# Kernel tuning notes

Hardware: AMD Instinct MI355X
Metric: run time of the kernel (lower is better)

The kernel has to match this reference:

```python
import jax, jax.numpy as jnp
import numpy as np

NUM_NODES = 50000
NUM_HYPEREDGES = 20000
NNZ = 1600000
IN_DIM = 256
OUT_DIM = 128


def setup_inputs() -> dict:
    key = jax.random.key(0)
    k1, k2, k3, k4, k5 = jax.random.split(key, 5)
    x = jax.random.normal(k1, (NUM_NODES, IN_DIM), dtype=jnp.float32)
    node_idx = jax.random.randint(k2, (NNZ,), 0, NUM_NODES)
    edge_idx = jax.random.randint(k3, (NNZ,), 0, NUM_HYPEREDGES)
    hyperedge_index = jnp.stack([node_idx, edge_idx], axis=0)  # [2, nnz]
    # glorot-style init for HypergraphConv's internal Linear (bias=False)
    scale = np.sqrt(6.0 / (IN_DIM + OUT_DIM)).astype(np.float32)
    lin_weight = jax.random.uniform(k4, (IN_DIM, OUT_DIM), dtype=jnp.float32,
                                    minval=-scale, maxval=scale)
    bias = jnp.zeros((OUT_DIM,), dtype=jnp.float32)
    return {"x_node_features": x, "lin_weight": lin_weight, "bias": bias,
            "hyperedge_index": hyperedge_index}


def reference(x_node_features, lin_weight, bias, hyperedge_index):
    src = hyperedge_index[0]   # node ids   [nnz]
    edge = hyperedge_index[1]  # hyperedge ids [nnz]
    ones = jnp.ones_like(src, dtype=x_node_features.dtype)

    # X Theta
    xw = x_node_features @ lin_weight  # [N, F_out]

    # D^{-1}: node degree (hyperedge weights default to 1)
    deg_n = jax.ops.segment_sum(ones, src, num_segments=NUM_NODES)
    d_inv = jnp.where(deg_n > 0, 1.0 / deg_n, 0.0)
    # B^{-1}: hyperedge cardinality
    deg_e = jax.ops.segment_sum(ones, edge, num_segments=NUM_HYPEREDGES)
    b_inv = jnp.where(deg_e > 0, 1.0 / deg_e, 0.0)

    # node -> hyperedge: m_e = B_e^{-1} * sum_{i in e} (X Theta)_i
    m_e = jax.ops.segment_sum(xw[src], edge, num_segments=NUM_HYPEREDGES)
    m_e = m_e * b_inv[:, None]  # [E, F_out]

    # hyperedge -> node: out_i = D_i^{-1} * sum_{e ni i} m_e
    out = jax.ops.segment_sum(m_e[edge], src, num_segments=NUM_NODES)
    out = out * d_inv[:, None] + bias  # [N, F_out]

    # ReLU + mean pool over nodes
    return jnp.mean(jax.nn.relu(out), axis=0)  # [F_out]
```

## Files before the change

kernel.cpp:

```cpp
#include <hip/hip_runtime.h>

#define NUM_N 50000
#define NUM_E 20000
#define IN_DIM 256
#define OUT_DIM 128
#define NBE 1250
#define NBN 1563
#define NCLS 8
#define ECAPC 256
#define NCAPC 192
#define SCAT_CHUNK 4096
#define NGEMM 782
#define XSCALE 16.0f

typedef unsigned short ushort_t;
typedef unsigned int uint_t;
typedef __attribute__((ext_vector_type(8))) short short8_t;
typedef __attribute__((ext_vector_type(4))) float f32x4_t;

__device__ __forceinline__ int clamp8(int q) { return min(max(q, -127), 127); }
__device__ __forceinline__ int lo8(uint_t u) { return (int)(signed char)(u & 0xff); }
__device__ __forceinline__ int hi8(uint_t u) { return ((int)(short)(ushort_t)u) >> 8; }
__device__ __forceinline__ ushort_t f2bf(float f) {
    uint_t u = __float_as_uint(f);
    u += 0x7fffu + ((u >> 16) & 1u);
    return (ushort_t)(u >> 16);
}

__global__ void init_kernel(int* __restrict__ gcur_e, int* __restrict__ gcur_n,
                            float* __restrict__ macc) {
    int t = blockIdx.x * 1024 + threadIdx.x;
    if (t < NCLS * NBE) gcur_e[t] = t * ECAPC;
    if (t < NCLS * NBN) gcur_n[t] = t * NCAPC;
    if (t < 128) macc[t] = 0.f;
}

__global__ __launch_bounds__(256) void gemm_scatter_kernel(
        const float* __restrict__ x, const float* __restrict__ w,
        char* __restrict__ xw, int nrows,
        const int* __restrict__ node_idx, const int* __restrict__ edge_idx, int nnz,
        int* __restrict__ gcur_e, int* __restrict__ gcur_n,
        uint_t* __restrict__ stag_e, uint_t* __restrict__ stag_n) {
    __shared__ int smem[5632];
    int tid = threadIdx.x;

    if (blockIdx.x >= NGEMM) {
        int* lh    = smem;
        int* lbase = smem + 2813;
        int cls = blockIdx.x & (NCLS - 1);
        int bid = blockIdx.x - NGEMM;
        int nblk = gridDim.x - NGEMM;
        for (int cbase = bid * SCAT_CHUNK; cbase < nnz; cbase += nblk * SCAT_CHUNK) {
            int cend = min(cbase + SCAT_CHUNK, nnz);
            for (int i = tid; i < NBE + NBN; i += 256) lh[i] = 0;
            __syncthreads();
            for (int i = cbase + tid; i < cend; i += 256) {
                atomicAdd(&lh[edge_idx[i] >> 4], 1);
                atomicAdd(&lh[NBE + (node_idx[i] >> 5)], 1);
            }
            __syncthreads();
            for (int i = tid; i < NBE; i += 256) {
                int c = lh[i];
                lbase[i] = c ? atomicAdd(&gcur_e[cls * NBE + i], c) : 0;
            }
            for (int i = tid; i < NBN; i += 256) {
                int c = lh[NBE + i];
                lbase[NBE + i] = c ? atomicAdd(&gcur_n[cls * NBN + i], c) : 0;
            }
            __syncthreads();
            for (int i = tid; i < NBE + NBN; i += 256) lh[i] = 0;
            __syncthreads();
            for (int i = cbase + tid; i < cend; i += 256) {
                int v = node_idx[i];
                int e = edge_idx[i];
                uint_t pk = ((uint_t)v << 16) | (uint_t)e;
                int be = e >> 4;
                int bn = v >> 5;
                int pe = lbase[be] + atomicAdd(&lh[be], 1);
                if (pe < (cls * NBE + be + 1) * ECAPC) stag_e[pe] = pk;
                int pn = lbase[NBE + bn] + atomicAdd(&lh[NBE + bn], 1);
                if (pn < (cls * NBN + bn + 1) * NCAPC) stag_n[pn] = pk;
            }
            __syncthreads();
        }
        return;
    }

    ushort_t* Wt = (ushort_t*)smem;
    int lane = tid & 63;
    int wv = tid >> 6;
    int R = blockIdx.x * 64 + wv * 16;
    int fr = lane & 15;
    int kb = lane >> 4;
    f32x4_t acc[8];
#pragma unroll
    for (int c = 0; c < 8; ++c) acc[c] = (f32x4_t){0.f, 0.f, 0.f, 0.f};
    int arow = min(R + fr, nrows - 1);
    const float* ap = x + (size_t)arow * IN_DIM + kb * 8;

    for (int k0 = 0; k0 < IN_DIM; k0 += 32) {
        __syncthreads();
        {
            int tk = tid >> 3;
            int tc = (tid & 7) * 16;
            const float* wp = w + (size_t)(k0 + tk) * OUT_DIM + tc;
            float4 w0 = *(const float4*)(wp + 0);
            float4 w1 = *(const float4*)(wp + 4);
            float4 w2 = *(const float4*)(wp + 8);
            float4 w3 = *(const float4*)(wp + 12);
            float wvv[16] = {w0.x, w0.y, w0.z, w0.w, w1.x, w1.y, w1.z, w1.w,
                             w2.x, w2.y, w2.z, w2.w, w3.x, w3.y, w3.z, w3.w};
#pragma unroll
            for (int i = 0; i < 16; ++i)
                Wt[(tc + i) * 40 + tk] = f2bf(wvv[i]);
        }
        __syncthreads();
        float4 a0 = *(const float4*)(ap + k0);
        float4 a1 = *(const float4*)(ap + k0 + 4);
        short8_t af;
        af[0] = (short)f2bf(a0.x); af[1] = (short)f2bf(a0.y);
        af[2] = (short)f2bf(a0.z); af[3] = (short)f2bf(a0.w);
        af[4] = (short)f2bf(a1.x); af[5] = (short)f2bf(a1.y);
        af[6] = (short)f2bf(a1.z); af[7] = (short)f2bf(a1.w);
#pragma unroll
        for (int c = 0; c < 8; ++c) {
            short8_t bf = *(short8_t*)&Wt[(c * 16 + fr) * 40 + kb * 8];
            acc[c] = __builtin_amdgcn_mfma_f32_16x16x32_bf16(af, bf, acc[c], 0, 0, 0);
        }
    }
#pragma unroll
    for (int c = 0; c < 8; ++c) {
#pragma unroll
        for (int j = 0; j < 4; ++j) {
            int row = R + kb * 4 + j;
            if (row < nrows) {
                int q = clamp8(__float2int_rn(acc[c][j] * XSCALE));
                xw[(size_t)row * OUT_DIM + c * 16 + fr] = (char)q;
            }
        }
    }
}

__global__ __launch_bounds__(256) void edge_agg_kernel(const uint_t* __restrict__ stag_e,
                                                       const int* __restrict__ gcur_e,
                                                       const ushort_t* __restrict__ xw16,
                                                       ushort_t* __restrict__ me16) {
    __shared__ int acc[16 * 128];
    __shared__ int cnt[16];
    int tid = threadIdx.x;
    int lane = tid & 63;
    int wid = tid >> 6;
    int b = blockIdx.x;
    for (int i = tid; i < 16 * 128; i += 256) acc[i] = 0;
    if (tid < 16) cnt[tid] = 0;
    __syncthreads();
#pragma unroll
    for (int ci = 0; ci < 2; ++ci) {
        int cls = wid + ci * 4;
        int idx = cls * NBE + b;
        int beg = idx * ECAPC;
        int end = min(gcur_e[idx], beg + ECAPC);
        int cb = beg;
        for (; cb + 16 <= end; cb += 16) {
            uint4 pa = *(const uint4*)&stag_e[cb];
            uint4 pb = *(const uint4*)&stag_e[cb + 4];
            uint4 pc = *(const uint4*)&stag_e[cb + 8];
            uint4 pd = *(const uint4*)&stag_e[cb + 12];
            uint_t pk[16] = {pa.x, pa.y, pa.z, pa.w, pb.x, pb.y, pb.z, pb.w,
                             pc.x, pc.y, pc.z, pc.w, pd.x, pd.y, pd.z, pd.w};
            uint_t u[16];
#pragma unroll
            for (int j = 0; j < 16; ++j)
                u[j] = xw16[(size_t)(pk[j] >> 16) * 64 + lane];
#pragma unroll
            for (int j = 0; j < 16; ++j) {
                int r = (pk[j] & 15) * 128;
                atomicAdd(&acc[r + lane],      lo8(u[j]));
                atomicAdd(&acc[r + 64 + lane], hi8(u[j]));
            }
            if (lane < 16) {
                uint_t p = stag_e[cb + lane];
                atomicAdd(&cnt[p & 15], 1);
            }
        }
        if (cb < end) {
            int m = end - cb;
            uint4 pa = *(const uint4*)&stag_e[cb];
            uint4 pb = *(const uint4*)&stag_e[cb + 4];
            uint4 pc = *(const uint4*)&stag_e[cb + 8];
            uint4 pd = *(const uint4*)&stag_e[cb + 12];
            uint_t pk[16] = {pa.x, pa.y, pa.z, pa.w, pb.x, pb.y, pb.z, pb.w,
                             pc.x, pc.y, pc.z, pc.w, pd.x, pd.y, pd.z, pd.w};
            uint_t u[16];
#pragma unroll
            for (int j = 0; j < 16; ++j)
                u[j] = xw16[(size_t)(pk[j] >> 16) * 64 + lane];
#pragma unroll
            for (int j = 0; j < 16; ++j) {
                bool ok = j < m;
                int r = (pk[j] & 15) * 128;
                atomicAdd(&acc[r + lane],      ok ? lo8(u[j]) : 0);
                atomicAdd(&acc[r + 64 + lane], ok ? hi8(u[j]) : 0);
            }
            if (lane < m) {
                uint_t p = stag_e[cb + lane];
                atomicAdd(&cnt[p & 15], 1);
            }
        }
    }
    __syncthreads();
    for (int r = wid; r < 16; r += 4) {
        int e = b * 16 + r;
        int c = cnt[r];
        float f = c ? 4.0f / (float)c : 0.f;
        int q0 = clamp8(__float2int_rn((float)acc[r * 128 + lane] * f));
        int q1 = clamp8(__float2int_rn((float)acc[r * 128 + 64 + lane] * f));
        me16[(size_t)e * 64 + lane] = (ushort_t)((q0 & 0xff) | ((q1 & 0xff) << 8));
    }
}

__global__ __launch_bounds__(256) void node_agg_kernel(const uint_t* __restrict__ stag_n,
                                                       const int* __restrict__ gcur_n,
                                                       const ushort_t* __restrict__ me16,
                                                       const float* __restrict__ bias,
                                                       float* __restrict__ mean_acc) {
    __shared__ int acc[32 * 128];
    __shared__ int cnt[32];
    int tid = threadIdx.x;
    int lane = tid & 63;
    int wid = tid >> 6;
    int b = blockIdx.x;
    for (int i = tid; i < 32 * 128; i += 256) acc[i] = 0;
    if (tid < 32) cnt[tid] = 0;
    __syncthreads();
#pragma unroll
    for (int ci = 0; ci < 2; ++ci) {
        int cls = wid + ci * 4;
        int idx = cls * NBN + b;
        int beg = idx * NCAPC;
        int end = min(gcur_n[idx], beg + NCAPC);
        int cb = beg;
        for (; cb + 16 <= end; cb += 16) {
            uint4 pa = *(const uint4*)&stag_n[cb];
            uint4 pb = *(const uint4*)&stag_n[cb + 4];
            uint4 pc = *(const uint4*)&stag_n[cb + 8];
            uint4 pd = *(const uint4*)&stag_n[cb + 12];
            uint_t pk[16] = {pa.x, pa.y, pa.z, pa.w, pb.x, pb.y, pb.z, pb.w,
                             pc.x, pc.y, pc.z, pc.w, pd.x, pd.y, pd.z, pd.w};
            uint_t u[16];
#pragma unroll
            for (int j = 0; j < 16; ++j)
                u[j] = me16[(size_t)(pk[j] & 0xffff) * 64 + lane];
#pragma unroll
            for (int j = 0; j < 16; ++j) {
                int r = ((pk[j] >> 16) & 31) * 128;
                atomicAdd(&acc[r + lane],      lo8(u[j]));
                atomicAdd(&acc[r + 64 + lane], hi8(u[j]));
            }
            if (lane < 16) {
                uint_t p = stag_n[cb + lane];
                atomicAdd(&cnt[(p >> 16) & 31], 1);
            }
        }
        if (cb < end) {
            int m = end - cb;
            uint4 pa = *(const uint4*)&stag_n[cb];
            uint4 pb = *(const uint4*)&stag_n[cb + 4];
            uint4 pc = *(const uint4*)&stag_n[cb + 8];
            uint4 pd = *(const uint4*)&stag_n[cb + 12];
            uint_t pk[16] = {pa.x, pa.y, pa.z, pa.w, pb.x, pb.y, pb.z, pb.w,
                             pc.x, pc.y, pc.z, pc.w, pd.x, pd.y, pd.z, pd.w};
            uint_t u[16];
#pragma unroll
            for (int j = 0; j < 16; ++j)
                u[j] = me16[(size_t)(pk[j] & 0xffff) * 64 + lane];
#pragma unroll
            for (int j = 0; j < 16; ++j) {
                bool ok = j < m;
                int r = ((pk[j] >> 16) & 31) * 128;
                atomicAdd(&acc[r + lane],      ok ? lo8(u[j]) : 0);
                atomicAdd(&acc[r + 64 + lane], ok ? hi8(u[j]) : 0);
            }
            if (lane < m) {
                uint_t p = stag_n[cb + lane];
                atomicAdd(&cnt[(p >> 16) & 31], 1);
            }
        }
    }
    __syncthreads();
    if (tid < 128) {
        int c = tid;
        int sw = (c & 1) ? (64 + (c >> 1)) : (c >> 1);
        float bc = bias[c];
        float s = 0.f;
        int nmax = min(32, NUM_N - b * 32);
        for (int r = 0; r < nmax; ++r) {
            int cc = cnt[r];
            float dinv = cc ? 1.0f / (64.0f * (float)cc) : 0.f;
            s += fmaxf((float)acc[r * 128 + sw] * dinv + bc, 0.f);
        }
        atomicAdd(&mean_acc[c], s);
    }
}

__global__ void finalize_kernel(const float* __restrict__ mean_acc, float* __restrict__ out) {
    int t = threadIdx.x;
    if (t < 128) out[t] = mean_acc[t] * (1.0f / (float)NUM_N);
}

extern "C" void kernel_launch(void* const* d_in, const int* in_sizes, int n_in,
                              void* d_out, int out_size, void* d_ws, size_t ws_size,
                              hipStream_t stream) {
    const float* x    = (const float*)d_in[0];
    const float* w    = (const float*)d_in[1];
    const float* bias = (const float*)d_in[2];
    const int*   hei  = (const int*)d_in[3];
    int nnz = in_sizes[3] / 2;
    const int* node_idx = hei;
    const int* edge_idx = hei + nnz;
    float* out = (float*)d_out;

    char* ws = (char*)d_ws;
    char*     xw     = ws;
    ushort_t* me16   = (ushort_t*)(ws + 6400000);
    uint_t*   stag_e = (uint_t*)(ws + 8960000);
    uint_t*   stag_n = (uint_t*)(ws + 19200064);
    int* gcur_e = (int*)(ws + 28803200);
    int* gcur_n = (int*)(ws + 28843200);
    float* macc = (float*)(ws + 28893216);

    int nscat = (nnz + SCAT_CHUNK - 1) / SCAT_CHUNK;

    init_kernel<<<13, 1024, 0, stream>>>(gcur_e, gcur_n, macc);
    gemm_scatter_kernel<<<NGEMM + nscat, 256, 0, stream>>>(
        x, w, xw, NUM_N, node_idx, edge_idx, nnz, gcur_e, gcur_n, stag_e, stag_n);

    edge_agg_kernel<<<NBE, 256, 0, stream>>>(stag_e, gcur_e, (const ushort_t*)xw, me16);
    node_agg_kernel<<<NBN, 256, 0, stream>>>(stag_n, gcur_n, me16, bias, macc);
    finalize_kernel<<<1, 128, 0, stream>>>(macc, out);
}
```

Baseline: 184.9 us.

## Replace LDS-histogram scatter with direct global atomic bucket placement

The scatter blocks no longer build a per-chunk shared-memory histogram, reserve ranges with one global atomic per bucket, and then place entries with LDS atomics. Each entry now takes its slot with a direct global atomicAdd on its class-partitioned bucket cursor, and the grid uses a fixed 392 scatter blocks. This removes four barriers and two passes over the indices per chunk, and cuts the shared memory per block, which may raise occupancy for the co-scheduled GEMM blocks. In exchange there are 3.2M global atomics with contention on hot cursors, and slot ordering inside a bucket becomes less local.

```diff
diff --git a/kernel.cpp b/kernel.cpp
--- a/kernel.cpp
+++ b/kernel.cpp
@@ -9,8 +9,8 @@
 #define NCLS 8
 #define ECAPC 256
 #define NCAPC 192
-#define SCAT_CHUNK 4096
 #define NGEMM 782
+#define NSCAT 392
 #define XSCALE 16.0f
 
 typedef unsigned short ushort_t;
@@ -41,47 +41,25 @@
         const int* __restrict__ node_idx, const int* __restrict__ edge_idx, int nnz,
         int* __restrict__ gcur_e, int* __restrict__ gcur_n,
         uint_t* __restrict__ stag_e, uint_t* __restrict__ stag_n) {
-    __shared__ int smem[5632];
+    __shared__ int smem[2560];
     int tid = threadIdx.x;
 
     if (blockIdx.x >= NGEMM) {
-        int* lh    = smem;
-        int* lbase = smem + 2813;
         int cls = blockIdx.x & (NCLS - 1);
         int bid = blockIdx.x - NGEMM;
-        int nblk = gridDim.x - NGEMM;
-        for (int cbase = bid * SCAT_CHUNK; cbase < nnz; cbase += nblk * SCAT_CHUNK) {
-            int cend = min(cbase + SCAT_CHUNK, nnz);
-            for (int i = tid; i < NBE + NBN; i += 256) lh[i] = 0;
-            __syncthreads();
-            for (int i = cbase + tid; i < cend; i += 256) {
-                atomicAdd(&lh[edge_idx[i] >> 4], 1);
-                atomicAdd(&lh[NBE + (node_idx[i] >> 5)], 1);
-            }
-            __syncthreads();
-            for (int i = tid; i < NBE; i += 256) {
-                int c = lh[i];
-                lbase[i] = c ? atomicAdd(&gcur_e[cls * NBE + i], c) : 0;
-            }
-            for (int i = tid; i < NBN; i += 256) {
-                int c = lh[NBE + i];
-                lbase[NBE + i] = c ? atomicAdd(&gcur_n[cls * NBN + i], c) : 0;
-            }
-            __syncthreads();
-            for (int i = tid; i < NBE + NBN; i += 256) lh[i] = 0;
-            __syncthreads();
-            for (int i = cbase + tid; i < cend; i += 256) {
-                int v = node_idx[i];
-                int e = edge_idx[i];
-                uint_t pk = ((uint_t)v << 16) | (uint_t)e;
-                int be = e >> 4;
-                int bn = v >> 5;
-                int pe = lbase[be] + atomicAdd(&lh[be], 1);
-                if (pe < (cls * NBE + be + 1) * ECAPC) stag_e[pe] = pk;
-                int pn = lbase[NBE + bn] + atomicAdd(&lh[NBE + bn], 1);
-                if (pn < (cls * NBN + bn + 1) * NCAPC) stag_n[pn] = pk;
-            }
-            __syncthreads();
+        int* ge = gcur_e + cls * NBE;
+        int* gn = gcur_n + cls * NBN;
+        int stride = NSCAT * 256;
+        for (int i = bid * 256 + tid; i < nnz; i += stride) {
+            int v = node_idx[i];
+            int e = edge_idx[i];
+            uint_t pk = ((uint_t)v << 16) | (uint_t)e;
+            int be = e >> 4;
+            int pe = atomicAdd(&ge[be], 1);
+            if (pe < (cls * NBE + be + 1) * ECAPC) stag_e[pe] = pk;
+            int bn = v >> 5;
+            int pn = atomicAdd(&gn[bn], 1);
+            if (pn < (cls * NBN + bn + 1) * NCAPC) stag_n[pn] = pk;
         }
         return;
     }
@@ -329,10 +307,8 @@
     int* gcur_n = (int*)(ws + 28843200);
     float* macc = (float*)(ws + 28893216);
 
-    int nscat = (nnz + SCAT_CHUNK - 1) / SCAT_CHUNK;
-
     init_kernel<<<13, 1024, 0, stream>>>(gcur_e, gcur_n, macc);
-    gemm_scatter_kernel<<<NGEMM + nscat, 256, 0, stream>>>(
+    gemm_scatter_kernel<<<NGEMM + NSCAT, 256, 0, stream>>>(
         x, w, xw, NUM_N, node_idx, edge_idx, nnz, gcur_e, gcur_n, stag_e, stag_n);
 
     edge_agg_kernel<<<NBE, 256, 0, stream>>>(stag_e, gcur_e, (const ushort_t*)xw, me16);
```

New measurement: 249.9 us. 1.35x slower.
